# Kernel tuning notes

Hardware: AMD Instinct MI355X
Metric: run time of the kernel (lower is better)

Reference implementation:

```python
import jax, jax.numpy as jnp
import numpy as np

B, S, D, K = 2048, 200, 64, 4  # batch, seq_len, dim, num_interest


def setup_inputs() -> dict:
    key = jax.random.key(0)
    k1, k2, k3, k4 = jax.random.split(key, 4)
    item_his_emb = jax.random.normal(k1, (B, S, D), dtype=jnp.float32)
    item_eb = jax.random.normal(k2, (B, D), dtype=jnp.float32)
    mask = jax.random.randint(k3, (B, S), 0, 2, dtype=jnp.int32)
    W = jax.random.normal(k4, (D, K * D), dtype=jnp.float32) * 0.05
    b = jnp.zeros((K * D,), dtype=jnp.float32)
    return {"item_his_emb": item_his_emb, "item_eb": item_eb, "mask": mask, "W": W, "b": b}


def _squash(v):
    # v: [B, K, D]; squash nonlinearity with the module's epsilon
    n2 = jnp.sum(jnp.square(v), axis=-1, keepdims=True)
    return (n2 / (1.0 + n2) / jnp.sqrt(n2 + 1e-9)) * v


def reference(item_his_emb, item_eb, mask, W, b):
    # bilinear_type == 1: Dense(dim * num_interest)
    hat = item_his_emb @ W + b                      # [B, S, K*D]
    hat = hat.reshape(B, S, K, D).transpose(0, 2, 1, 3)  # [B, K, S, D]

    mask_zero = (mask == 0)[:, None, :]             # [B, 1, S] broadcast over K
    cw = jnp.zeros((B, K, S), dtype=item_his_emb.dtype)

    interest = None
    for i in range(3):
        sw = jax.nn.softmax(cw, axis=1)             # softmax over interests
        sw = jnp.where(mask_zero, 0.0, sw)          # [B, K, S]
        interest = _squash(jnp.einsum('bks,bksd->bkd', sw, hat))  # [B, K, D]
        if i < 2:
            cw = cw + jnp.einsum('bksd,bkd->bks', hat, interest)

    # readout: softmax attention over interests against target item, hard argmax gather
    atten = jax.nn.softmax(jnp.einsum('bkd,bd->bk', interest, item_eb), axis=1)
    idx = jnp.argmax(atten, axis=1)                 # [B]
    readout = jnp.take_along_axis(interest, idx[:, None, None], axis=1)[:, 0, :]  # [B, D]
    return interest, readout
```

## Files before the change

kernel.cpp:

```cpp
#include <hip/hip_runtime.h>


#define NB 2048
#define NS 200
#define ND 64
#define NK 4
#define NT 512

__device__ __forceinline__ int rot(int s) { return (s + (s >> 3)) & 15; }

__device__ __forceinline__ void gload16(const float* g_, float* l_) {
  __builtin_amdgcn_global_load_lds(
      (const __attribute__((address_space(1))) unsigned int*)g_,
      (__attribute__((address_space(3))) unsigned int*)l_, 16, 0, 0);
}

template <int CTRL>
__device__ __forceinline__ float dppadd(float v) {
  int p = __builtin_amdgcn_update_dpp(0, __float_as_int(v), CTRL, 0xF, 0xF, true);
  return v + __int_as_float(p);
}

#if __has_builtin(__builtin_amdgcn_permlane16_swap)
__device__ __forceinline__ float pl16add(float v) {
  auto r = __builtin_amdgcn_permlane16_swap(__float_as_int(v), __float_as_int(v),
                                            false, false);
  return __int_as_float(r[0]) + __int_as_float(r[1]);
}
#else
__device__ __forceinline__ float pl16add(float v) { return v + __shfl_xor(v, 16, 64); }
#endif

#if __has_builtin(__builtin_amdgcn_permlane32_swap)
__device__ __forceinline__ float pl32add(float v) {
  auto r = __builtin_amdgcn_permlane32_swap(__float_as_int(v), __float_as_int(v),
                                            false, false);
  return __int_as_float(r[0]) + __int_as_float(r[1]);
}
#else
__device__ __forceinline__ float pl32add(float v) { return v + __shfl_xor(v, 32, 64); }
#endif

__device__ __forceinline__ float red_j(float v) {
  v = dppadd<0x124>(v);
  v = dppadd<0x128>(v);
  v = pl16add(v);
  v = pl32add(v);
  return v;
}
__device__ __forceinline__ float red_q(float v) {
  v = dppadd<0xB1>(v);
  v = dppadd<0x4E>(v);
  return v;
}
__device__ __forceinline__ float red64(float v) { return red_j(red_q(v)); }

__global__ __launch_bounds__(NT, 2) void caps_kernel(
    const float* __restrict__ his, const float* __restrict__ itemeb,
    const int* __restrict__ mask, const float* __restrict__ W,
    const float* __restrict__ bias, float* __restrict__ out) {
  __shared__ float semb[NS * ND];
  __shared__ float pe[8][NK][ND];
  __shared__ float sG[NK][ND];
  __shared__ float su[NK][ND];
  __shared__ float spv[NK][ND];
  __shared__ float smsk[NS];
  __shared__ float4 pts4[8];
  __shared__ __align__(16) float soff[NK];
  __shared__ float satt[NK];
  __shared__ int sidx;

  const int t = threadIdx.x;
  const int w = t >> 6, l = t & 63;
  const int g = l & 3, j = l >> 2;
  const int gid = (w << 2) | g;
  const int ke = w & 3, h_ = w >> 2;
  const int b = blockIdx.x;
  const float* eb = his + (size_t)b * NS * ND;

  float wreg[32];
#pragma unroll
  for (int c = 0; c < 32; ++c)
    wreg[c] = W[(size_t)(32 * h_ + c) * (NK * ND) + ke * ND + l];
  float breg = bias[ke * ND + l];
  float iq = itemeb[(size_t)b * ND + l];

  {
    const int sg = l >> 4, sj = l & 15;
    for (int i = w; i < 50; i += 8) {
      int s = 4 * i + sg;
      int q = (sj - rot(s)) & 15;
      gload16(eb + (s << 6) + (q << 2), &semb[i * 256]);
    }
  }
  if (t < NS) smsk[t] = (mask[(size_t)b * NS + t] != 0) ? 1.0f : 0.0f;
  __syncthreads();

  const int ntr = (w < 2) ? 7 : 6;

  for (int it = 0; it < 3; ++it) {
    float4 a0 = {0, 0, 0, 0}, a1 = {0, 0, 0, 0}, a2 = {0, 0, 0, 0},
           a3 = {0, 0, 0, 0};
    float t0 = 0, t1 = 0, t2 = 0, t3 = 0;

    if (it == 0) {
      for (int tt = 0; tt < ntr; ++tt) {
        int s = gid + 32 * tt;
        float4 eq = *(const float4*)&semb[(s << 6) + 4 * ((j + rot(s)) & 15)];
        float sw = 0.25f * smsk[s];
        a0.x += sw * eq.x; a0.y += sw * eq.y;
        a0.z += sw * eq.z; a0.w += sw * eq.w;
        t0 += sw;
      }
      a0.x = red_q(a0.x); a0.y = red_q(a0.y);
      a0.z = red_q(a0.z); a0.w = red_q(a0.w);
      t0 = red_q(t0);
      a1 = a0; a2 = a0; a3 = a0; t1 = t0; t2 = t0; t3 = t0;
    } else {
      float4 u0 = *(const float4*)&su[0][4 * j];
      float4 u1 = *(const float4*)&su[1][4 * j];
      float4 u2 = *(const float4*)&su[2][4 * j];
      float4 u3 = *(const float4*)&su[3][4 * j];
      float4 sof = *(const float4*)&soff[0];
      for (int tt = 0; tt < ntr; ++tt) {
        int s = gid + 32 * tt;
        float4 eq = *(const float4*)&semb[(s << 6) + 4 * ((j + rot(s)) & 15)];
        float mk = smsk[s];
        float lg0 = eq.x * u0.x + eq.y * u0.y + eq.z * u0.z + eq.w * u0.w;
        float lg1 = eq.x * u1.x + eq.y * u1.y + eq.z * u1.z + eq.w * u1.w;
        float lg2 = eq.x * u2.x + eq.y * u2.y + eq.z * u2.z + eq.w * u2.w;
        float lg3 = eq.x * u3.x + eq.y * u3.y + eq.z * u3.z + eq.w * u3.w;
        lg0 = red_j(lg0) + sof.x;
        lg1 = red_j(lg1) + sof.y;
        lg2 = red_j(lg2) + sof.z;
        lg3 = red_j(lg3) + sof.w;
        float mx = fmaxf(fmaxf(lg0, lg1), fmaxf(lg2, lg3));
        float e0 = __expf(lg0 - mx), e1 = __expf(lg1 - mx);
        float e2 = __expf(lg2 - mx), e3 = __expf(lg3 - mx);
        float r = mk / (e0 + e1 + e2 + e3);
        float sw0 = e0 * r, sw1 = e1 * r, sw2 = e2 * r, sw3 = e3 * r;
        a0.x += sw0 * eq.x; a0.y += sw0 * eq.y; a0.z += sw0 * eq.z; a0.w += sw0 * eq.w;
        a1.x += sw1 * eq.x; a1.y += sw1 * eq.y; a1.z += sw1 * eq.z; a1.w += sw1 * eq.w;
        a2.x += sw2 * eq.x; a2.y += sw2 * eq.y; a2.z += sw2 * eq.z; a2.w += sw2 * eq.w;
        a3.x += sw3 * eq.x; a3.y += sw3 * eq.y; a3.z += sw3 * eq.z; a3.w += sw3 * eq.w;
        t0 += sw0; t1 += sw1; t2 += sw2; t3 += sw3;
      }
      a0.x = red_q(a0.x); a0.y = red_q(a0.y); a0.z = red_q(a0.z); a0.w = red_q(a0.w);
      a1.x = red_q(a1.x); a1.y = red_q(a1.y); a1.z = red_q(a1.z); a1.w = red_q(a1.w);
      a2.x = red_q(a2.x); a2.y = red_q(a2.y); a2.z = red_q(a2.z); a2.w = red_q(a2.w);
      a3.x = red_q(a3.x); a3.y = red_q(a3.y); a3.z = red_q(a3.z); a3.w = red_q(a3.w);
      t0 = red_q(t0); t1 = red_q(t1); t2 = red_q(t2); t3 = red_q(t3);
    }
    if (g == 0) {
      *(float4*)&pe[w][0][4 * j] = a0;
      *(float4*)&pe[w][1][4 * j] = a1;
      *(float4*)&pe[w][2][4 * j] = a2;
      *(float4*)&pe[w][3][4 * j] = a3;
    }
    if (l == 0) pts4[w] = make_float4(t0, t1, t2, t3);
    __syncthreads();

    {
      int cl = 32 * h_ + (l & 31);
      float sse = 0.f;
#pragma unroll
      for (int w2 = 0; w2 < 8; ++w2) sse += pe[w2][ke][cl];
      su[ke][cl] = sse;
      float vp = 0.f;
#pragma unroll
      for (int q2 = 0; q2 < 8; ++q2) {
        float4 e4 = *(const float4*)&su[ke][32 * h_ + 4 * q2];
        vp += e4.x * wreg[4 * q2 + 0] + e4.y * wreg[4 * q2 + 1] +
              e4.z * wreg[4 * q2 + 2] + e4.w * wreg[4 * q2 + 3];
      }
      if (h_) spv[ke][l] = vp;
      __syncthreads();

      if (h_ == 0) {
        float ts_ = 0.f;
#pragma unroll
        for (int w2 = 0; w2 < 8; ++w2) ts_ += ((const float*)&pts4[w2])[ke];
        float accv = vp + spv[ke][l] + ts_ * breg;
        float n2 = red64(accv * accv);
        float scale = n2 / (1.f + n2) / sqrtf(n2 + 1e-9f);
        float inter = scale * accv;
        if (it < 2) {
          float gnew = (it == 0) ? inter : (sG[ke][l] + inter);
          sG[ke][l] = gnew;
          float ob = red64(breg * gnew);
          if (l == 0) soff[ke] = ob;
          const float4* Wr =
              (const float4*)(W + (size_t)l * (NK * ND) + ke * ND);
          const float4* Gk = (const float4*)&sG[ke][0];
          float a = 0.f;
#pragma unroll
          for (int d4 = 0; d4 < 16; ++d4) {
            float4 wv = Wr[d4], gv = Gk[d4];
            a += wv.x * gv.x + wv.y * gv.y + wv.z * gv.z + wv.w * gv.w;
          }
          su[ke][l] = a;
        } else {
          out[((size_t)b * NK + ke) * ND + l] = inter;
          float dot_ = red64(inter * iq);
          spv[ke][l] = inter;
          if (l == 0) satt[ke] = dot_;
        }
      }
      __syncthreads();
    }
  }

  if (t == 0) {
    int bi = 0;
    float bv = satt[0];
#pragma unroll
    for (int kk = 1; kk < NK; ++kk)
      if (satt[kk] > bv) { bv = satt[kk]; bi = kk; }
    sidx = bi;
  }
  __syncthreads();
  if (t < ND) out[(size_t)NB * NK * ND + (size_t)b * ND + t] = spv[sidx][t];
}

extern "C" void kernel_launch(void* const* d_in, const int* in_sizes, int n_in,
                              void* d_out, int out_size, void* d_ws, size_t ws_size,
                              hipStream_t stream) {
  (void)in_sizes; (void)n_in; (void)out_size; (void)d_ws; (void)ws_size;
  const float* his = (const float*)d_in[0];
  const float* itemeb = (const float*)d_in[1];
  const int* mask = (const int*)d_in[2];
  const float* W = (const float*)d_in[3];
  const float* bias = (const float*)d_in[4];
  float* out = (float*)d_out;
  caps_kernel<<<NB, NT, 0, stream>>>(his, itemeb, mask, W, bias, out);
}
```

Before: 88.94 us.

## Split squash and W-projection across both half-warpgroups, fold log2e into logits

The per-iteration squash and the W·G projection used to run on only half the waves (h_==0) while the other half idled. Both halves now compute the squash redundantly, and each half computes half of the projection dot product into separate su2 buffers that are summed when read. This removes one idle phase and some serial work per iteration. The change also pre-scales the logits by log2(e) so exp2f can replace __expf, keeps the running G in a register, and stores the mask as bytes. The cost is duplicated squash reductions and an extra add when the su2 halves are read.

```diff
diff --git a/kernel.cpp b/kernel.cpp
--- a/kernel.cpp
+++ b/kernel.cpp
@@ -6,6 +6,7 @@
 #define ND 64
 #define NK 4
 #define NT 512
+#define LOG2E 1.44269504f
 
 __device__ __forceinline__ int rot(int s) { return (s + (s >> 3)) & 15; }
 
@@ -61,11 +62,11 @@
     const float* __restrict__ bias, float* __restrict__ out) {
   __shared__ float semb[NS * ND];
   __shared__ float pe[8][NK][ND];
+  __shared__ float su2[2][NK][ND];
+  __shared__ float spv2[2][NK][ND];
   __shared__ float sG[NK][ND];
-  __shared__ float su[NK][ND];
-  __shared__ float spv[NK][ND];
-  __shared__ float smsk[NS];
   __shared__ float4 pts4[8];
+  __shared__ unsigned char smsk8[NS];
   __shared__ __align__(16) float soff[NK];
   __shared__ float satt[NK];
   __shared__ int sidx;
@@ -93,10 +94,11 @@
       gload16(eb + (s << 6) + (q << 2), &semb[i * 256]);
     }
   }
-  if (t < NS) smsk[t] = (mask[(size_t)b * NS + t] != 0) ? 1.0f : 0.0f;
+  if (t < NS) smsk8[t] = (mask[(size_t)b * NS + t] != 0) ? 1 : 0;
   __syncthreads();
 
   const int ntr = (w < 2) ? 7 : 6;
+  float greg = 0.f;
 
   for (int it = 0; it < 3; ++it) {
     float4 a0 = {0, 0, 0, 0}, a1 = {0, 0, 0, 0}, a2 = {0, 0, 0, 0},
@@ -107,7 +109,7 @@
       for (int tt = 0; tt < ntr; ++tt) {
         int s = gid + 32 * tt;
         float4 eq = *(const float4*)&semb[(s << 6) + 4 * ((j + rot(s)) & 15)];
-        float sw = 0.25f * smsk[s];
+        float sw = 0.25f * (float)smsk8[s];
         a0.x += sw * eq.x; a0.y += sw * eq.y;
         a0.z += sw * eq.z; a0.w += sw * eq.w;
         t0 += sw;
@@ -117,15 +119,26 @@
       t0 = red_q(t0);
       a1 = a0; a2 = a0; a3 = a0; t1 = t0; t2 = t0; t3 = t0;
     } else {
-      float4 u0 = *(const float4*)&su[0][4 * j];
-      float4 u1 = *(const float4*)&su[1][4 * j];
-      float4 u2 = *(const float4*)&su[2][4 * j];
-      float4 u3 = *(const float4*)&su[3][4 * j];
+      float4 u0, u1, u2, u3;
+      {
+        float4 p0 = *(const float4*)&su2[0][0][4 * j];
+        float4 q0 = *(const float4*)&su2[1][0][4 * j];
+        u0 = make_float4(p0.x + q0.x, p0.y + q0.y, p0.z + q0.z, p0.w + q0.w);
+        float4 p1 = *(const float4*)&su2[0][1][4 * j];
+        float4 q1 = *(const float4*)&su2[1][1][4 * j];
+        u1 = make_float4(p1.x + q1.x, p1.y + q1.y, p1.z + q1.z, p1.w + q1.w);
+        float4 p2 = *(const float4*)&su2[0][2][4 * j];
+        float4 q2 = *(const float4*)&su2[1][2][4 * j];
+        u2 = make_float4(p2.x + q2.x, p2.y + q2.y, p2.z + q2.z, p2.w + q2.w);
+        float4 p3 = *(const float4*)&su2[0][3][4 * j];
+        float4 q3 = *(const float4*)&su2[1][3][4 * j];
+        u3 = make_float4(p3.x + q3.x, p3.y + q3.y, p3.z + q3.z, p3.w + q3.w);
+      }
       float4 sof = *(const float4*)&soff[0];
       for (int tt = 0; tt < ntr; ++tt) {
         int s = gid + 32 * tt;
         float4 eq = *(const float4*)&semb[(s << 6) + 4 * ((j + rot(s)) & 15)];
-        float mk = smsk[s];
+        float mk = (float)smsk8[s];
         float lg0 = eq.x * u0.x + eq.y * u0.y + eq.z * u0.z + eq.w * u0.w;
         float lg1 = eq.x * u1.x + eq.y * u1.y + eq.z * u1.z + eq.w * u1.w;
         float lg2 = eq.x * u2.x + eq.y * u2.y + eq.z * u2.z + eq.w * u2.w;
@@ -135,8 +148,8 @@
         lg2 = red_j(lg2) + sof.z;
         lg3 = red_j(lg3) + sof.w;
         float mx = fmaxf(fmaxf(lg0, lg1), fmaxf(lg2, lg3));
-        float e0 = __expf(lg0 - mx), e1 = __expf(lg1 - mx);
-        float e2 = __expf(lg2 - mx), e3 = __expf(lg3 - mx);
+        float e0 = exp2f(lg0 - mx), e1 = exp2f(lg1 - mx);
+        float e2 = exp2f(lg2 - mx), e3 = exp2f(lg3 - mx);
         float r = mk / (e0 + e1 + e2 + e3);
         float sw0 = e0 * r, sw1 = e1 * r, sw2 = e2 * r, sw3 = e3 * r;
         a0.x += sw0 * eq.x; a0.y += sw0 * eq.y; a0.z += sw0 * eq.z; a0.w += sw0 * eq.w;
@@ -165,49 +178,49 @@
       float sse = 0.f;
 #pragma unroll
       for (int w2 = 0; w2 < 8; ++w2) sse += pe[w2][ke][cl];
-      su[ke][cl] = sse;
+      su2[0][ke][cl] = sse;
       float vp = 0.f;
 #pragma unroll
       for (int q2 = 0; q2 < 8; ++q2) {
-        float4 e4 = *(const float4*)&su[ke][32 * h_ + 4 * q2];
+        float4 e4 = *(const float4*)&su2[0][ke][32 * h_ + 4 * q2];
         vp += e4.x * wreg[4 * q2 + 0] + e4.y * wreg[4 * q2 + 1] +
               e4.z * wreg[4 * q2 + 2] + e4.w * wreg[4 * q2 + 3];
       }
-      if (h_) spv[ke][l] = vp;
-      __syncthreads();
-
-      if (h_ == 0) {
-        float ts_ = 0.f;
-#pragma unroll
-        for (int w2 = 0; w2 < 8; ++w2) ts_ += ((const float*)&pts4[w2])[ke];
-        float accv = vp + spv[ke][l] + ts_ * breg;
-        float n2 = red64(accv * accv);
-        float scale = n2 / (1.f + n2) / sqrtf(n2 + 1e-9f);
-        float inter = scale * accv;
-        if (it < 2) {
-          float gnew = (it == 0) ? inter : (sG[ke][l] + inter);
-          sG[ke][l] = gnew;
-          float ob = red64(breg * gnew);
-          if (l == 0) soff[ke] = ob;
-          const float4* Wr =
-              (const float4*)(W + (size_t)l * (NK * ND) + ke * ND);
-          const float4* Gk = (const float4*)&sG[ke][0];
-          float a = 0.f;
-#pragma unroll
-          for (int d4 = 0; d4 < 16; ++d4) {
-            float4 wv = Wr[d4], gv = Gk[d4];
-            a += wv.x * gv.x + wv.y * gv.y + wv.z * gv.z + wv.w * gv.w;
-          }
-          su[ke][l] = a;
-        } else {
-          out[((size_t)b * NK + ke) * ND + l] = inter;
-          float dot_ = red64(inter * iq);
-          spv[ke][l] = inter;
-          if (l == 0) satt[ke] = dot_;
+      spv2[h_][ke][l] = vp;
+    }
+    __syncthreads();
+
+    {
+      float ts_ = 0.f;
+#pragma unroll
+      for (int w2 = 0; w2 < 8; ++w2) ts_ += ((const float*)&pts4[w2])[ke];
+      float accv = spv2[0][ke][l] + spv2[1][ke][l] + ts_ * breg;
+      float n2 = red64(accv * accv);
+      float scale = n2 / (1.f + n2) / sqrtf(n2 + 1e-9f);
+      float inter = scale * accv;
+      if (it < 2) {
+        greg += inter;
+        sG[ke][l] = greg;
+        float ob = red64(breg * greg);
+        if (h_ == 0 && l == 0) soff[ke] = ob * LOG2E;
+        const float4* Wr =
+            (const float4*)(W + (size_t)l * (NK * ND) + ke * ND + 32 * h_);
+        const float4* Gk = (const float4*)&sG[ke][32 * h_];
+        float a = 0.f;
+#pragma unroll
+        for (int d4 = 0; d4 < 8; ++d4) {
+          float4 wv = Wr[d4], gv = Gk[d4];
+          a += wv.x * gv.x + wv.y * gv.y + wv.z * gv.z + wv.w * gv.w;
         }
-      }
-      __syncthreads();
-    }
+        su2[h_][ke][l] = LOG2E * a;
+      } else if (h_ == 0) {
+        out[((size_t)b * NK + ke) * ND + l] = inter;
+        float dot_ = red64(inter * iq);
+        pe[0][ke][l] = inter;
+        if (l == 0) satt[ke] = dot_;
+      }
+    }
+    __syncthreads();
   }
 
   if (t == 0) {
@@ -219,7 +232,7 @@
     sidx = bi;
   }
   __syncthreads();
-  if (t < ND) out[(size_t)NB * NK * ND + (size_t)b * ND + t] = spv[sidx][t];
+  if (t < ND) out[(size_t)NB * NK * ND + (size_t)b * ND + t] = pe[0][sidx][t];
 }
 
 extern "C" void kernel_launch(void* const* d_in, const int* in_sizes, int n_in,
```

Result: slower. 93.79 us (+5.5%).
